# Optimization experiments

Measured on AMD Instinct MI355X. Metric: run time of the kernel, lower is better.

The kernel has to match this reference:

```python
import jax, jax.numpy as jnp
import numpy as np

B, S, D, H, HS = 2, 2048, 1024, 16, 64


def setup_inputs() -> dict:
    key = jax.random.key(0)
    ks = jax.random.split(key, 4)
    x = jax.random.normal(ks[0], (B, S, D), dtype=jnp.float32)
    # causal mask: 1.0 where key_pos <= query_pos, else 0.0
    mask = jnp.tril(jnp.ones((S, S), dtype=jnp.float32))
    w_qkv = jax.random.normal(ks[1], (D, 3, H, HS), dtype=jnp.float32) * 0.02
    b_qkv = jnp.zeros((3, H, HS), dtype=jnp.float32)
    w_proj = jax.random.normal(ks[2], (H, HS, D), dtype=jnp.float32) * 0.02
    b_proj = jnp.zeros((D,), dtype=jnp.float32)
    return {"x": x, "mask": mask, "w_qkv": w_qkv, "b_qkv": b_qkv,
            "w_proj": w_proj, "b_proj": b_proj}


def reference(x, mask, w_qkv, b_qkv, w_proj, b_proj):
    # c_attn: [B,S,D] @ [D,3,H,HS] -> [B,S,3,H,HS]
    qkv = jnp.einsum('bsd,dthc->bsthc', x, w_qkv) + b_qkv
    q, k, v = qkv[:, :, 0], qkv[:, :, 1], qkv[:, :, 2]  # [B,S,H,HS]
    scale = jax.lax.rsqrt(float(HS))
    q = q * scale
    # scores over head_size: [B,H,S(query),S(key)]
    scores = jnp.einsum('bqhc,bkhc->bhqk', q, k)
    scores = scores + (1.0 - mask) * -1e9
    weights = jax.nn.softmax(scores, axis=-1).astype(x.dtype)
    # attn_pdrop = 0.0 / inference: dropout is identity
    attn = jnp.einsum('bhqk,bkhc->bqhc', weights, v)  # [B,S,H,HS]
    out = jnp.einsum('bqhc,hcd->bqd', attn, w_proj) + b_proj
    return out
```

## Files before the change

kernel.cpp:

```cpp
#include <hip/hip_runtime.h>
#include <hip/hip_bf16.h>


#define Bb 2
#define Ss 2048
#define Dd 1024
#define Hh 16
#define HSs 64

typedef __bf16 bf16x8 __attribute__((ext_vector_type(8)));
typedef float  f32x4  __attribute__((ext_vector_type(4)));

__device__ __forceinline__ unsigned short f2bf(float f) {
  unsigned int u = __float_as_uint(f);
  unsigned int lsb = (u >> 16) & 1u;
  u += 0x7fffu + lsb;
  return (unsigned short)(u >> 16);
}

__device__ __forceinline__ void async16(const unsigned short* g, unsigned short* l) {
  __builtin_amdgcn_global_load_lds(
      (const __attribute__((address_space(1))) unsigned int*)g,
      (__attribute__((address_space(3))) unsigned int*)l,
      16, 0, 0);
}

__global__ __launch_bounds__(256) void k_cvt_bf16(const float* __restrict__ in,
                                                  unsigned short* __restrict__ out,
                                                  int n) {
  int i = (blockIdx.x * 256 + threadIdx.x) * 4;
  int stride = gridDim.x * 256 * 4;
  for (; i < n; i += stride) {
    float4 v = *reinterpret_cast<const float4*>(in + i);
    ushort4 o;
    o.x = f2bf(v.x); o.y = f2bf(v.y); o.z = f2bf(v.z); o.w = f2bf(v.w);
    *reinterpret_cast<ushort4*>(out + i) = o;
  }
}

__global__ __launch_bounds__(256) void k_transpose_bf16(const float* __restrict__ in,
                                                        unsigned short* __restrict__ out,
                                                        int R, int C) {
  __shared__ float t[32][33];
  int c0 = blockIdx.x * 32, r0 = blockIdx.y * 32;
  int tx = threadIdx.x, ty = threadIdx.y;
  #pragma unroll
  for (int i = 0; i < 32; i += 8)
    t[ty + i][tx] = in[(size_t)(r0 + ty + i) * C + (c0 + tx)];
  __syncthreads();
  #pragma unroll
  for (int i = 0; i < 32; i += 8)
    out[(size_t)(c0 + ty + i) * R + (r0 + tx)] = f2bf(t[tx][ty + i]);
}

__global__ __launch_bounds__(256) void k_gemm_qkv(const unsigned short* __restrict__ A,
                                                  const unsigned short* __restrict__ Bt,
                                                  const float* __restrict__ bias,
                                                  unsigned short* __restrict__ Qg,
                                                  unsigned short* __restrict__ Kg,
                                                  unsigned short* __restrict__ Vt) {
  __shared__ unsigned short S[2][128 * 64];
  const int K = 1024;
  int bid = blockIdx.x;
  int swz = (bid % 8) * 96 + bid / 8;
  int tm = swz / 24, tn = swz % 24;
  int m0 = tm * 128, n0 = tn * 128;
  int tid = threadIdx.x;
  int w = tid >> 6, l = tid & 63;
  int lr = l & 15, lg = l >> 4;
  int wm = (w >> 1) * 64, wn = (w & 1) * 64;
  int srow = l >> 3, scol = (l & 7) * 8;

  f32x4 acc[4][4];
  #pragma unroll
  for (int i = 0; i < 4; ++i)
    #pragma unroll
    for (int j = 0; j < 4; ++j)
      acc[i][j] = (f32x4){0.f, 0.f, 0.f, 0.f};

  for (int k0 = 0; k0 < K; k0 += 64) {
    #pragma unroll
    for (int c = 0; c < 4; ++c) {
      int chunk = w * 4 + c;
      int row = chunk * 8 + srow;
      async16(&A[(size_t)(m0 + row) * K + k0 + scol], &S[0][chunk * 512]);
      async16(&Bt[(size_t)(n0 + row) * K + k0 + scol], &S[1][chunk * 512]);
    }
    __syncthreads();
    #pragma unroll
    for (int kk = 0; kk < 64; kk += 32) {
      bf16x8 af[4], bfr[4];
      #pragma unroll
      for (int mf = 0; mf < 4; ++mf)
        af[mf] = *reinterpret_cast<const bf16x8*>(&S[0][(wm + mf * 16 + lr) * 64 + kk + lg * 8]);
      #pragma unroll
      for (int nf = 0; nf < 4; ++nf)
        bfr[nf] = *reinterpret_cast<const bf16x8*>(&S[1][(wn + nf * 16 + lr) * 64 + kk + lg * 8]);
      #pragma unroll
      for (int mf = 0; mf < 4; ++mf)
        #pragma unroll
        for (int nf = 0; nf < 4; ++nf)
          acc[mf][nf] = __builtin_amdgcn_mfma_f32_16x16x32_bf16(af[mf], bfr[nf], acc[mf][nf], 0, 0, 0);
    }
    __syncthreads();
  }

  if (n0 < 2048) {
    #pragma unroll
    for (int mf = 0; mf < 4; ++mf) {
      #pragma unroll
      for (int nf = 0; nf < 4; ++nf) {
        int n = n0 + wn + nf * 16 + lr;
        int t = n >> 10, r = n & 1023;
        int h = r >> 6, cc = r & 63;
        float bv = bias[n];
        #pragma unroll
        for (int j = 0; j < 4; ++j) {
          int m = m0 + wm + mf * 16 + lg * 4 + j;
          int b = m >> 11, s = m & 2047;
          size_t idx = ((size_t)(b * Hh + h) * Ss + s) * HSs + cc;
          float v = acc[mf][nf][j] + bv;
          if (t == 0) Qg[idx] = f2bf(v * 0.1803368801111244f);
          else        Kg[idx] = f2bf(v);
        }
      }
    }
  } else {
    unsigned short* Ts = &S[0][0];
    #pragma unroll
    for (int mf = 0; mf < 4; ++mf)
      #pragma unroll
      for (int nf = 0; nf < 4; ++nf) {
        int nl = wn + nf * 16 + lr;
        float bv = bias[n0 + nl];
        #pragma unroll
        for (int j = 0; j < 4; ++j) {
          int ml = wm + mf * 16 + lg * 4 + j;
          Ts[nl * 128 + (ml ^ ((nl & 7) << 3))] = f2bf(acc[mf][nf][j] + bv);
        }
      }
    __syncthreads();
    int nl = tid >> 1, mh = (tid & 1) * 64;
    int n = n0 + nl;
    int h = (n & 1023) >> 6, cc = n & 63;
    int bb = m0 >> 11, s0 = m0 & 2047;
    unsigned short* dst = &Vt[((size_t)(bb * Hh + h) * HSs + cc) * Ss + s0];
    #pragma unroll
    for (int i = 0; i < 8; ++i) {
      int m = mh + i * 8;
      bf16x8 v = *reinterpret_cast<const bf16x8*>(&Ts[nl * 128 + (m ^ ((nl & 7) << 3))]);
      *reinterpret_cast<bf16x8*>(&dst[m]) = v;
    }
  }
}

__global__ __launch_bounds__(512, 4) void k_attn(const unsigned short* __restrict__ Qg,
                                                 const unsigned short* __restrict__ Kg,
                                                 const unsigned short* __restrict__ Vt,
                                                 unsigned short* __restrict__ Ob) {
  __shared__ unsigned short Ks[128 * 64];
  __shared__ unsigned short Vs[64 * 128];
  __shared__ unsigned short Ps[8][16 * 128];

  int bid = blockIdx.x;
  int c = bid >> 8, bh = (bid >> 3) & 31, p = bid & 7;
  int qt = c ? (15 - p) : p;
  int b = bh >> 4, h = bh & 15;
  int qs0 = qt * 128;

  int tid = threadIdx.x;
  int w = tid >> 6, l = tid & 63;
  int lr = l & 15, lg = l >> 4;
  int qw = qs0 + w * 16;
  int srow = l >> 3, scolK = (l & 7) * 8;
  int rrV = l >> 4, colV = (l & 15) * 8;

  bf16x8 qf[2];
  #pragma unroll
  for (int kx = 0; kx < 2; ++kx)
    qf[kx] = *reinterpret_cast<const bf16x8*>(
        &Qg[((size_t)bh * Ss + qw + lr) * HSs + kx * 32 + lg * 8]);

  f32x4 oacc[4];
  #pragma unroll
  for (int nf = 0; nf < 4; ++nf) oacc[nf] = (f32x4){0.f, 0.f, 0.f, 0.f};
  float mrun[4], lrun[4];
  #pragma unroll
  for (int j = 0; j < 4; ++j) { mrun[j] = -1e30f; lrun[j] = 0.f; }

  int ntiles = qt + 1;
  for (int t = 0; t < ntiles; ++t) {
    #pragma unroll
    for (int cc = 0; cc < 2; ++cc) {
      int ch = w * 2 + cc;
      int rowK = ch * 8 + srow;
      int swK = scolK ^ ((srow & 7) << 3);
      async16(&Kg[((size_t)bh * Ss + t * 128 + rowK) * HSs + swK], &Ks[ch * 512]);
      int rowV = ch * 4 + rrV;
      int swV = colV ^ ((rowV & 7) << 3);
      async16(&Vt[((size_t)bh * HSs + rowV) * Ss + t * 128 + swV], &Vs[ch * 512]);
    }
    __syncthreads();

    f32x4 sacc[8];
    #pragma unroll
    for (int nf = 0; nf < 8; ++nf) sacc[nf] = (f32x4){0.f, 0.f, 0.f, 0.f};
    #pragma unroll
    for (int kx = 0; kx < 2; ++kx) {
      #pragma unroll
      for (int nf = 0; nf < 8; ++nf) {
        int rk = nf * 16 + lr;
        bf16x8 kf = *reinterpret_cast<const bf16x8*>(
            &Ks[rk * 64 + ((kx * 32 + lg * 8) ^ ((rk & 7) << 3))]);
        sacc[nf] = __builtin_amdgcn_mfma_f32_16x16x32_bf16(qf[kx], kf, sacc[nf], 0, 0, 0);
      }
    }

    if (t == qt) {
      #pragma unroll
      for (int nf = 0; nf < 8; ++nf) {
        int kcol = qs0 + nf * 16 + lr;
        #pragma unroll
        for (int j = 0; j < 4; ++j) {
          int qg2 = qw + lg * 4 + j;
          if (kcol > qg2) sacc[nf][j] = -1e30f;
        }
      }
    }

    float rmax[4];
    #pragma unroll
    for (int j = 0; j < 4; ++j) {
      float rm = fmaxf(fmaxf(fmaxf(sacc[0][j], sacc[1][j]), fmaxf(sacc[2][j], sacc[3][j])),
                       fmaxf(fmaxf(sacc[4][j], sacc[5][j]), fmaxf(sacc[6][j], sacc[7][j])));
      #pragma unroll
      for (int d = 1; d < 16; d <<= 1)
        rm = fmaxf(rm, __shfl_xor(rm, d));
      rmax[j] = rm;
    }
    bool need = (rmax[0] > mrun[0] + 8.f) | (rmax[1] > mrun[1] + 8.f) |
                (rmax[2] > mrun[2] + 8.f) | (rmax[3] > mrun[3] + 8.f);
    if (__any(need)) {
      #pragma unroll
      for (int j = 0; j < 4; ++j) {
        float mnew = fmaxf(mrun[j], rmax[j]);
        float cf = exp2f(mrun[j] - mnew);
        mrun[j] = mnew;
        lrun[j] *= cf;
        #pragma unroll
        for (int nf = 0; nf < 4; ++nf)
          oacc[nf][j] *= cf;
      }
    }
    #pragma unroll
    for (int j = 0; j < 4; ++j) {
      float psum = 0.f;
      #pragma unroll
      for (int nf = 0; nf < 8; ++nf) {
        float pv = exp2f(sacc[nf][j] - mrun[j]);
        sacc[nf][j] = pv;
        psum += pv;
      }
      #pragma unroll
      for (int d = 1; d < 16; d <<= 1)
        psum += __shfl_xor(psum, d);
      lrun[j] += psum;
    }

    #pragma unroll
    for (int nf = 0; nf < 8; ++nf)
      #pragma unroll
      for (int j = 0; j < 4; ++j) {
        int prow = lg * 4 + j;
        Ps[w][prow * 128 + ((nf * 16 + lr) ^ ((prow & 7) << 3))] = f2bf(sacc[nf][j]);
      }

    #pragma unroll
    for (int kx = 0; kx < 4; ++kx) {
      bf16x8 pf = *reinterpret_cast<const bf16x8*>(
          &Ps[w][lr * 128 + ((kx * 32 + lg * 8) ^ ((lr & 7) << 3))]);
      #pragma unroll
      for (int nf = 0; nf < 4; ++nf) {
        int rv = nf * 16 + lr;
        bf16x8 vf = *reinterpret_cast<const bf16x8*>(
            &Vs[rv * 128 + ((kx * 32 + lg * 8) ^ ((rv & 7) << 3))]);
        oacc[nf] = __builtin_amdgcn_mfma_f32_16x16x32_bf16(pf, vf, oacc[nf], 0, 0, 0);
      }
    }
    __syncthreads();
  }

  #pragma unroll
  for (int j = 0; j < 4; ++j) {
    float rinv = 1.0f / lrun[j];
    int s = qw + lg * 4 + j;
    #pragma unroll
    for (int nf = 0; nf < 4; ++nf) {
      int cc = nf * 16 + lr;
      Ob[((size_t)(b * Ss + s)) * Dd + h * HSs + cc] = f2bf(oacc[nf][j] * rinv);
    }
  }
}

__global__ __launch_bounds__(256) void k_gemm_out(const unsigned short* __restrict__ A,
                                                  const unsigned short* __restrict__ Bt,
                                                  const float* __restrict__ bias,
                                                  float* __restrict__ Out) {
  __shared__ unsigned short As[128 * 64];
  __shared__ unsigned short Bs[128 * 64];
  const int K = 1024;
  int bid = blockIdx.x;
  int swz = (bid % 8) * 32 + bid / 8;
  int tm = swz / 8, tn = swz % 8;
  int m0 = tm * 128, n0 = tn * 128;
  int tid = threadIdx.x;
  int w = tid >> 6, l = tid & 63;
  int lr = l & 15, lg = l >> 4;
  int wm = (w >> 1) * 64, wn = (w & 1) * 64;
  int srow = l >> 3, scol = (l & 7) * 8;

  f32x4 acc[4][4];
  #pragma unroll
  for (int i = 0; i < 4; ++i)
    #pragma unroll
    for (int j = 0; j < 4; ++j)
      acc[i][j] = (f32x4){0.f, 0.f, 0.f, 0.f};

  for (int k0 = 0; k0 < K; k0 += 64) {
    #pragma unroll
    for (int c = 0; c < 4; ++c) {
      int chunk = w * 4 + c;
      int row = chunk * 8 + srow;
      async16(&A[(size_t)(m0 + row) * K + k0 + scol], &As[chunk * 512]);
      async16(&Bt[(size_t)(n0 + row) * K + k0 + scol], &Bs[chunk * 512]);
    }
    __syncthreads();
    #pragma unroll
    for (int kk = 0; kk < 64; kk += 32) {
      bf16x8 af[4], bfr[4];
      #pragma unroll
      for (int mf = 0; mf < 4; ++mf)
        af[mf] = *reinterpret_cast<const bf16x8*>(&As[(wm + mf * 16 + lr) * 64 + kk + lg * 8]);
      #pragma unroll
      for (int nf = 0; nf < 4; ++nf)
        bfr[nf] = *reinterpret_cast<const bf16x8*>(&Bs[(wn + nf * 16 + lr) * 64 + kk + lg * 8]);
      #pragma unroll
      for (int mf = 0; mf < 4; ++mf)
        #pragma unroll
        for (int nf = 0; nf < 4; ++nf)
          acc[mf][nf] = __builtin_amdgcn_mfma_f32_16x16x32_bf16(af[mf], bfr[nf], acc[mf][nf], 0, 0, 0);
    }
    __syncthreads();
  }

  #pragma unroll
  for (int mf = 0; mf < 4; ++mf)
    #pragma unroll
    for (int nf = 0; nf < 4; ++nf) {
      int n = n0 + wn + nf * 16 + lr;
      float bv = bias[n];
      #pragma unroll
      for (int j = 0; j < 4; ++j) {
        int m = m0 + wm + mf * 16 + lg * 4 + j;
        Out[(size_t)m * 1024 + n] = acc[mf][nf][j] + bv;
      }
    }
}

extern "C" void kernel_launch(void* const* d_in, const int* in_sizes, int n_in,
                              void* d_out, int out_size, void* d_ws, size_t ws_size,
                              hipStream_t stream) {
  (void)in_sizes; (void)n_in; (void)out_size; (void)ws_size;
  const float* x      = (const float*)d_in[0];
  const float* w_qkv  = (const float*)d_in[2];
  const float* b_qkv  = (const float*)d_in[3];
  const float* w_proj = (const float*)d_in[4];
  const float* b_proj = (const float*)d_in[5];
  float* out = (float*)d_out;

  char* ws = (char*)d_ws;
  unsigned short* xb    = (unsigned short*)(ws);
  unsigned short* wqkvT = (unsigned short*)(ws + 8388608);
  unsigned short* wpT   = (unsigned short*)(ws + 14680064);
  unsigned short* Qg    = (unsigned short*)(ws + 16777216);
  unsigned short* Kg    = (unsigned short*)(ws + 25165824);
  unsigned short* Vt    = (unsigned short*)(ws + 33554432);
  unsigned short* attnb = (unsigned short*)(ws + 41943040);

  k_cvt_bf16<<<dim3(2048), dim3(256), 0, stream>>>(x, xb, Bb * Ss * Dd);
  k_transpose_bf16<<<dim3(96, 32), dim3(32, 8), 0, stream>>>(w_qkv, wqkvT, 1024, 3072);
  k_transpose_bf16<<<dim3(32, 32), dim3(32, 8), 0, stream>>>(w_proj, wpT, 1024, 1024);
  k_gemm_qkv<<<dim3(32 * 24), dim3(256), 0, stream>>>(xb, wqkvT, b_qkv, Qg, Kg, Vt);
  k_attn<<<dim3(512), dim3(512), 0, stream>>>(Qg, Kg, Vt, attnb);
  k_gemm_out<<<dim3(32 * 8), dim3(256), 0, stream>>>(attnb, wpT, b_proj, out);
}
```

Measured before the change: 259.3 us.

## Restructure attention into 64-row tiles, paired causal blocks, double-buffered K/V

The attention kernel now uses 64-query tiles with 4 waves per block. Each block processes a pair of query tiles (q and 31-q), so every block runs the same 33 key tiles and the causal work is balanced. K/V tiles are double-buffered, with the next tile's async load issued before computing the current one, which removes one barrier per iteration. The cost is more K/V tile loads per query row because the tiles are smaller, plus extra per-tile softmax bookkeeping.

```diff
diff --git a/kernel.cpp b/kernel.cpp
--- a/kernel.cpp
+++ b/kernel.cpp
@@ -154,32 +154,35 @@
   }
 }
 
-__global__ __launch_bounds__(512, 4) void k_attn(const unsigned short* __restrict__ Qg,
+__global__ __launch_bounds__(256, 4) void k_attn(const unsigned short* __restrict__ Qg,
                                                  const unsigned short* __restrict__ Kg,
                                                  const unsigned short* __restrict__ Vt,
                                                  unsigned short* __restrict__ Ob) {
-  __shared__ unsigned short Ks[128 * 64];
-  __shared__ unsigned short Vs[64 * 128];
-  __shared__ unsigned short Ps[8][16 * 128];
+  __shared__ unsigned short Ks[2][64 * 64];
+  __shared__ unsigned short Vs[2][64 * 64];
+  __shared__ unsigned short Ps[4][16 * 64];
 
   int bid = blockIdx.x;
-  int c = bid >> 8, bh = (bid >> 3) & 31, p = bid & 7;
-  int qt = c ? (15 - p) : p;
+  int q = bid >> 5, bh = bid & 31;
   int b = bh >> 4, h = bh & 15;
-  int qs0 = qt * 128;
+  int qtA = q, qtB = 31 - q;
+  int ntA = qtA + 1;
 
   int tid = threadIdx.x;
   int w = tid >> 6, l = tid & 63;
   int lr = l & 15, lg = l >> 4;
-  int qw = qs0 + w * 16;
-  int srow = l >> 3, scolK = (l & 7) * 8;
-  int rrV = l >> 4, colV = (l & 15) * 8;
-
+  int srow = l >> 3, scol = (l & 7) * 8;
+  int swcol = scol ^ (srow << 3);
+
+  const size_t kbase = (size_t)bh * Ss;
+  const size_t vbase = (size_t)bh * HSs;
+
+  int qt = qtA, qs0 = qtA * 64, qw = qs0 + w * 16;
   bf16x8 qf[2];
   #pragma unroll
   for (int kx = 0; kx < 2; ++kx)
     qf[kx] = *reinterpret_cast<const bf16x8*>(
-        &Qg[((size_t)bh * Ss + qw + lr) * HSs + kx * 32 + lg * 8]);
+        &Qg[(kbase + qw + lr) * HSs + kx * 32 + lg * 8]);
 
   f32x4 oacc[4];
   #pragma unroll
@@ -188,38 +191,74 @@
   #pragma unroll
   for (int j = 0; j < 4; ++j) { mrun[j] = -1e30f; lrun[j] = 0.f; }
 
-  int ntiles = qt + 1;
-  for (int t = 0; t < ntiles; ++t) {
-    #pragma unroll
-    for (int cc = 0; cc < 2; ++cc) {
-      int ch = w * 2 + cc;
-      int rowK = ch * 8 + srow;
-      int swK = scolK ^ ((srow & 7) << 3);
-      async16(&Kg[((size_t)bh * Ss + t * 128 + rowK) * HSs + swK], &Ks[ch * 512]);
-      int rowV = ch * 4 + rrV;
-      int swV = colV ^ ((rowV & 7) << 3);
-      async16(&Vt[((size_t)bh * HSs + rowV) * Ss + t * 128 + swV], &Vs[ch * 512]);
-    }
-    __syncthreads();
-
-    f32x4 sacc[8];
-    #pragma unroll
-    for (int nf = 0; nf < 8; ++nf) sacc[nf] = (f32x4){0.f, 0.f, 0.f, 0.f};
+  auto stage = [&](int tile, int buf) {
+    #pragma unroll
+    for (int cch = 0; cch < 2; ++cch) {
+      int rr = w * 16 + cch * 8 + srow;
+      async16(&Kg[(kbase + tile * 64 + rr) * HSs + swcol], &Ks[buf][(w * 2 + cch) * 512]);
+      async16(&Vt[(vbase + rr) * Ss + tile * 64 + swcol], &Vs[buf][(w * 2 + cch) * 512]);
+    }
+  };
+
+  auto writeO = [&]() {
+    #pragma unroll
+    for (int j = 0; j < 4; ++j) {
+      float rinv = 1.0f / lrun[j];
+      int s = qw + lg * 4 + j;
+      #pragma unroll
+      for (int nf = 0; nf < 4; ++nf) {
+        int cc = nf * 16 + lr;
+        Ob[((size_t)(b * Ss + s)) * Dd + h * HSs + cc] = f2bf(oacc[nf][j] * rinv);
+      }
+    }
+  };
+
+  stage(0, 0);
+
+  for (int g = 0; g < 33; ++g) {
+    __syncthreads();
+
+    if (g + 1 < 33) {
+      int nt = g + 1;
+      int tile = (nt < ntA) ? nt : (nt - ntA);
+      stage(tile, (g + 1) & 1);
+    }
+
+    if (g == ntA) {
+      writeO();
+      qt = qtB; qs0 = qtB * 64; qw = qs0 + w * 16;
+      #pragma unroll
+      for (int kx = 0; kx < 2; ++kx)
+        qf[kx] = *reinterpret_cast<const bf16x8*>(
+            &Qg[(kbase + qw + lr) * HSs + kx * 32 + lg * 8]);
+      #pragma unroll
+      for (int nf = 0; nf < 4; ++nf) oacc[nf] = (f32x4){0.f, 0.f, 0.f, 0.f};
+      #pragma unroll
+      for (int j = 0; j < 4; ++j) { mrun[j] = -1e30f; lrun[j] = 0.f; }
+    }
+
+    int t = (g < ntA) ? g : g - ntA;
+    int cur = g & 1;
+
+    f32x4 sacc[4];
+    #pragma unroll
+    for (int nf = 0; nf < 4; ++nf) sacc[nf] = (f32x4){0.f, 0.f, 0.f, 0.f};
     #pragma unroll
     for (int kx = 0; kx < 2; ++kx) {
-      #pragma unroll
-      for (int nf = 0; nf < 8; ++nf) {
-        int rk = nf * 16 + lr;
-        bf16x8 kf = *reinterpret_cast<const bf16x8*>(
-            &Ks[rk * 64 + ((kx * 32 + lg * 8) ^ ((rk & 7) << 3))]);
-        sacc[nf] = __builtin_amdgcn_mfma_f32_16x16x32_bf16(qf[kx], kf, sacc[nf], 0, 0, 0);
-      }
+      bf16x8 kf[4];
+      #pragma unroll
+      for (int nf = 0; nf < 4; ++nf)
+        kf[nf] = *reinterpret_cast<const bf16x8*>(
+            &Ks[cur][(nf * 16 + lr) * 64 + ((kx * 32 + lg * 8) ^ ((lr & 7) << 3))]);
+      #pragma unroll
+      for (int nf = 0; nf < 4; ++nf)
+        sacc[nf] = __builtin_amdgcn_mfma_f32_16x16x32_bf16(qf[kx], kf[nf], sacc[nf], 0, 0, 0);
     }
 
     if (t == qt) {
       #pragma unroll
-      for (int nf = 0; nf < 8; ++nf) {
-        int kcol = qs0 + nf * 16 + lr;
+      for (int nf = 0; nf < 4; ++nf) {
+        int kcol = t * 64 + nf * 16 + lr;
         #pragma unroll
         for (int j = 0; j < 4; ++j) {
           int qg2 = qw + lg * 4 + j;
@@ -231,8 +270,7 @@
     float rmax[4];
     #pragma unroll
     for (int j = 0; j < 4; ++j) {
-      float rm = fmaxf(fmaxf(fmaxf(sacc[0][j], sacc[1][j]), fmaxf(sacc[2][j], sacc[3][j])),
-                       fmaxf(fmaxf(sacc[4][j], sacc[5][j]), fmaxf(sacc[6][j], sacc[7][j])));
+      float rm = fmaxf(fmaxf(sacc[0][j], sacc[1][j]), fmaxf(sacc[2][j], sacc[3][j]));
       #pragma unroll
       for (int d = 1; d < 16; d <<= 1)
         rm = fmaxf(rm, __shfl_xor(rm, d));
@@ -256,7 +294,7 @@
     for (int j = 0; j < 4; ++j) {
       float psum = 0.f;
       #pragma unroll
-      for (int nf = 0; nf < 8; ++nf) {
+      for (int nf = 0; nf < 4; ++nf) {
         float pv = exp2f(sacc[nf][j] - mrun[j]);
         sacc[nf][j] = pv;
         psum += pv;
@@ -268,38 +306,29 @@
     }
 
     #pragma unroll
-    for (int nf = 0; nf < 8; ++nf)
+    for (int nf = 0; nf < 4; ++nf)
       #pragma unroll
       for (int j = 0; j < 4; ++j) {
         int prow = lg * 4 + j;
-        Ps[w][prow * 128 + ((nf * 16 + lr) ^ ((prow & 7) << 3))] = f2bf(sacc[nf][j]);
-      }
-
-    #pragma unroll
-    for (int kx = 0; kx < 4; ++kx) {
+        Ps[w][prow * 64 + ((nf * 16 + lr) ^ ((prow & 7) << 3))] = f2bf(sacc[nf][j]);
+      }
+
+    #pragma unroll
+    for (int kx = 0; kx < 2; ++kx) {
       bf16x8 pf = *reinterpret_cast<const bf16x8*>(
-          &Ps[w][lr * 128 + ((kx * 32 + lg * 8) ^ ((lr & 7) << 3))]);
-      #pragma unroll
-      for (int nf = 0; nf < 4; ++nf) {
-        int rv = nf * 16 + lr;
-        bf16x8 vf = *reinterpret_cast<const bf16x8*>(
-            &Vs[rv * 128 + ((kx * 32 + lg * 8) ^ ((rv & 7) << 3))]);
-        oacc[nf] = __builtin_amdgcn_mfma_f32_16x16x32_bf16(pf, vf, oacc[nf], 0, 0, 0);
-      }
-    }
-    __syncthreads();
+          &Ps[w][lr * 64 + ((kx * 32 + lg * 8) ^ ((lr & 7) << 3))]);
+      bf16x8 vf[4];
+      #pragma unroll
+      for (int nf = 0; nf < 4; ++nf)
+        vf[nf] = *reinterpret_cast<const bf16x8*>(
+            &Vs[cur][(nf * 16 + lr) * 64 + ((kx * 32 + lg * 8) ^ ((lr & 7) << 3))]);
+      #pragma unroll
+      for (int nf = 0; nf < 4; ++nf)
+        oacc[nf] = __builtin_amdgcn_mfma_f32_16x16x32_bf16(pf, vf[nf], oacc[nf], 0, 0, 0);
+    }
   }
 
-  #pragma unroll
-  for (int j = 0; j < 4; ++j) {
-    float rinv = 1.0f / lrun[j];
-    int s = qw + lg * 4 + j;
-    #pragma unroll
-    for (int nf = 0; nf < 4; ++nf) {
-      int cc = nf * 16 + lr;
-      Ob[((size_t)(b * Ss + s)) * Dd + h * HSs + cc] = f2bf(oacc[nf][j] * rinv);
-    }
-  }
+  writeO();
 }
 
 __global__ __launch_bounds__(256) void k_gemm_out(const unsigned short* __restrict__ A,
@@ -391,6 +420,6 @@
   k_transpose_bf16<<<dim3(96, 32), dim3(32, 8), 0, stream>>>(w_qkv, wqkvT, 1024, 3072);
   k_transpose_bf16<<<dim3(32, 32), dim3(32, 8), 0, stream>>>(w_proj, wpT, 1024, 1024);
   k_gemm_qkv<<<dim3(32 * 24), dim3(256), 0, stream>>>(xb, wqkvT, b_qkv, Qg, Kg, Vt);
-  k_attn<<<dim3(512), dim3(512), 0, stream>>>(Qg, Kg, Vt, attnb);
+  k_attn<<<dim3(512), dim3(256), 0, stream>>>(Qg, Kg, Vt, attnb);
   k_gemm_out<<<dim3(32 * 8), dim3(256), 0, stream>>>(attnb, wpT, b_proj, out);
 }
```

Result: faster. 245.3 us (-5.4%).
